# Kernel tuning notes

Measured on AMD Instinct MI355X. Metric: run time of the kernel, lower is better.

The kernel has to match this reference:

```python
import jax, jax.numpy as jnp
import numpy as np

N_NODES = 100000
N_ANGLES = 1000000
SCALAR_DIM = 128
ANGLE_ATTR_DIM = 2
HIDDEN = 64


def setup_inputs() -> dict:
    key = jax.random.key(0)
    ks = jax.random.split(key, 10)
    x = jax.random.normal(ks[0], (N_NODES, SCALAR_DIM), dtype=jnp.float32)
    triple_index = jax.random.randint(ks[1], (3, N_ANGLES), 0, N_NODES, dtype=jnp.int64)
    triple_attr = jax.random.normal(ks[2], (N_ANGLES, ANGLE_ATTR_DIM), dtype=jnp.float32)
    d_in = SCALAR_DIM * 2 + ANGLE_ATTR_DIM  # 258
    W1 = jax.random.normal(ks[3], (d_in, HIDDEN), dtype=jnp.float32) / np.sqrt(d_in)
    b1 = jnp.zeros((HIDDEN,), dtype=jnp.float32)
    W2 = jax.random.normal(ks[4], (HIDDEN, HIDDEN), dtype=jnp.float32) / np.sqrt(HIDDEN)
    b2 = jnp.zeros((HIDDEN,), dtype=jnp.float32)
    W3 = jax.random.normal(ks[5], (HIDDEN, SCALAR_DIM), dtype=jnp.float32) / np.sqrt(HIDDEN)
    b3 = jnp.zeros((SCALAR_DIM,), dtype=jnp.float32)
    # o3.Linear 128x0e -> 128x0e: bias-free dense linear with 1/sqrt(fan_in) norm
    Wout = jax.random.normal(ks[6], (SCALAR_DIM, SCALAR_DIM), dtype=jnp.float32) / np.sqrt(SCALAR_DIM)
    return {"x": x, "triple_index": triple_index, "triple_attr": triple_attr,
            "W1": W1, "b1": b1, "W2": W2, "b2": b2, "W3": W3, "b3": b3, "Wout": Wout}


def reference(x, triple_index, triple_attr, W1, b1, W2, b2, W3, b3, Wout):
    num_nodes = x.shape[0]
    x_scalar = x[:, :SCALAR_DIM]
    i, j, k = triple_index[0], triple_index[1], triple_index[2]
    # gather endpoints, concat with angle attrs: [E, 2*scalar_dim + 2]
    angle_input = jnp.concatenate([x_scalar[i], x_scalar[k], triple_attr], axis=-1)
    h = jax.nn.silu(angle_input @ W1 + b1)
    h = jax.nn.silu(h @ W2 + b2)
    msgs = h @ W3 + b3  # [E, scalar_dim]
    # scatter-mean by j
    sums = jax.ops.segment_sum(msgs, j, num_segments=num_nodes)
    cnts = jax.ops.segment_sum(jnp.ones((msgs.shape[0],), msgs.dtype), j, num_segments=num_nodes)
    aggr = sums / jnp.maximum(cnts, 1.0)[:, None]
    return aggr @ Wout
```

## Files before the change

kernel.cpp:

```cpp
#include <hip/hip_runtime.h>

#define NN 100000
#define NE 1000000
#define NBLK_SCAN 391

typedef float f4 __attribute__((ext_vector_type(4)));
typedef float f2 __attribute__((ext_vector_type(2)));
typedef _Float16 h8 __attribute__((ext_vector_type(8)));

__device__ __forceinline__ float silu(float v) {
    return v / (1.0f + __expf(-v));
}

#define O_SUMS   0
#define O_CNT    6400000
#define O_OFF    6500000
#define O_BSUM   6600000
#define O_PERM   6600512
#define O_XA     7600512
#define O_XB     10800512
#define O_W3W    14000512
#define O_W2T    14008832
#define O_W1TH   14010880
#define O_W1TR   14019072

#define HIST_B  3907
#define W3W_B   33
#define PREP0_B (HIST_B + W3W_B + 1 + 8)
#define NPRE_B  1563
#define MID_B   (NPRE_B + NBLK_SCAN)

__global__ __launch_bounds__(256) void k_prep0(
    const int* __restrict__ tj,
    const float* __restrict__ W1, const float* __restrict__ W2,
    const float* __restrict__ W3, const float* __restrict__ b3,
    const float* __restrict__ Wout,
    int* __restrict__ C, float* __restrict__ W3W, _Float16* __restrict__ W2t,
    _Float16* __restrict__ W1th, _Float16* __restrict__ W1tr) {
    const int b = blockIdx.x;
    const int t = threadIdx.x;
    if (b < HIST_B) {
        int e = b * 256 + t;
        if (e < NE) atomicAdd(&C[__builtin_nontemporal_load(tj + e)], 1);
    } else if (b < HIST_B + W3W_B) {
        const int row = (b - HIST_B) * 2 + (t >> 7);
        const int c = t & 127;
        if (row < 65) {
            const float* arow = (row < 64) ? (W3 + row * 128) : b3;
            float acc = 0.f;
            for (int d = 0; d < 128; ++d) acc += arow[d] * Wout[d * 128 + c];
            W3W[row * 128 + c] = acc;
        }
    } else if (b < HIST_B + W3W_B + 1) {
#pragma unroll
        for (int u = 0; u < 16; ++u) {
            const int idx = t * 16 + u;
            const int n = idx >> 6, k = idx & 63;
            W2t[idx] = (_Float16)W2[k * 64 + n];
        }
    } else {
        const int b0 = b - (HIST_B + W3W_B + 1);
#pragma unroll
        for (int u = 0; u < 8; ++u) {
            const int idx = b0 * 2048 + t * 8 + u;
            const int np = idx >> 7, k = idx & 127;
            const float wfull = W1[(k + ((np >= 64) ? 128 : 0)) * 64 + (np & 63)];
            const _Float16 wh = (_Float16)wfull;
            W1th[idx] = wh;
            W1tr[idx] = (_Float16)(wfull - (float)wh);
        }
    }
}

__global__ __launch_bounds__(256) void k_mid(
    const float* __restrict__ x,
    const _Float16* __restrict__ W1th, const _Float16* __restrict__ W1tr,
    _Float16* __restrict__ XA, _Float16* __restrict__ XB,
    const int* __restrict__ C, float* __restrict__ sums,
    int* __restrict__ offv, int* __restrict__ Bsum) {
    __shared__ _Float16 XOUT[2][64][72];
    __shared__ int s[256];
    const int b = blockIdx.x;
    const int t = threadIdx.x;
    if (b < NPRE_B) {
        const int n0 = b * 64;
        const int w = t >> 6;
        const int lane = t & 63;
        const int r15 = lane & 15, blk = lane >> 4;
        const int nodeRow = n0 + w * 16 + r15;
        const bool rowOK = nodeRow < NN;
        f4 accA[4], accB[4];
#pragma unroll
        for (int n = 0; n < 4; ++n) {
            accA[n] = (f4){0.f, 0.f, 0.f, 0.f};
            accB[n] = (f4){0.f, 0.f, 0.f, 0.f};
        }
#pragma unroll
        for (int kk = 0; kk < 4; ++kk) {
            f4 x0 = (f4){0.f, 0.f, 0.f, 0.f}, x1 = x0;
            if (rowOK) {
                const f4* xp = (const f4*)(x + (size_t)nodeRow * 128 + kk * 32 + blk * 8);
                x0 = xp[0];
                x1 = xp[1];
            }
            h8 xh, xr;
#pragma unroll
            for (int n = 0; n < 4; ++n) {
                xh[n] = (_Float16)x0[n];
                xr[n] = (_Float16)(x0[n] - (float)xh[n]);
                xh[4 + n] = (_Float16)x1[n];
                xr[4 + n] = (_Float16)(x1[n] - (float)xh[4 + n]);
            }
#pragma unroll
            for (int ncol = 0; ncol < 4; ++ncol) {
                const int nA = ncol * 16 + r15;
                const int koff = kk * 32 + blk * 8;
                h8 whA = *(const h8*)(W1th + nA * 128 + koff);
                h8 wrA = *(const h8*)(W1tr + nA * 128 + koff);
                accA[ncol] = __builtin_amdgcn_mfma_f32_16x16x32_f16(xh, whA, accA[ncol], 0, 0, 0);
                accA[ncol] = __builtin_amdgcn_mfma_f32_16x16x32_f16(xr, whA, accA[ncol], 0, 0, 0);
                accA[ncol] = __builtin_amdgcn_mfma_f32_16x16x32_f16(xh, wrA, accA[ncol], 0, 0, 0);
                h8 whB = *(const h8*)(W1th + (64 + nA) * 128 + koff);
                h8 wrB = *(const h8*)(W1tr + (64 + nA) * 128 + koff);
                accB[ncol] = __builtin_amdgcn_mfma_f32_16x16x32_f16(xh, whB, accB[ncol], 0, 0, 0);
                accB[ncol] = __builtin_amdgcn_mfma_f32_16x16x32_f16(xr, whB, accB[ncol], 0, 0, 0);
                accB[ncol] = __builtin_amdgcn_mfma_f32_16x16x32_f16(xh, wrB, accB[ncol], 0, 0, 0);
            }
        }
#pragma unroll
        for (int ncol = 0; ncol < 4; ++ncol)
#pragma unroll
            for (int reg = 0; reg < 4; ++reg) {
                const int row = w * 16 + blk * 4 + reg;
                XOUT[0][row][ncol * 16 + r15] = (_Float16)accA[ncol][reg];
                XOUT[1][row][ncol * 16 + r15] = (_Float16)accB[ncol][reg];
            }
        __syncthreads();
#pragma unroll
        for (int u = 0; u < 4; ++u) {
            const int idx = t + 256 * u;
            const int mat = idx >> 9;
            const int row = (idx >> 3) & 63;
            const int c8 = idx & 7;
            const int grow = n0 + row;
            if (grow < NN) {
                _Float16* dst = (mat ? XB : XA) + (size_t)grow * 64 + c8 * 8;
                *(h8*)dst = *(const h8*)&XOUT[mat][row][c8 * 8];
            }
        }
    } else {
        const int sb = b - NPRE_B;
        {
            f4* sz = (f4*)sums + (size_t)sb * 4096;
            const int cnt4 = min(4096, 1600000 - sb * 4096);
            for (int u = t; u < cnt4; u += 256) sz[u] = (f4){0.f, 0.f, 0.f, 0.f};
        }
        const int gid = sb * 256 + t;
        const int v = (gid < NN) ? C[gid] : 0;
        s[t] = v;
        __syncthreads();
        for (int off = 1; off < 256; off <<= 1) {
            int add = (t >= off) ? s[t - off] : 0;
            __syncthreads();
            s[t] += add;
            __syncthreads();
        }
        if (gid < NN) offv[gid] = s[t] - v;
        if (t == 255) Bsum[sb] = s[255];
    }
}

__global__ __launch_bounds__(256) void k_scatter(const int* __restrict__ tj,
                                                 const int* __restrict__ Bsum,
                                                 int* __restrict__ offv,
                                                 int* __restrict__ perm) {
    __shared__ int BpreS[NBLK_SCAN];
    const int t = threadIdx.x;
    const int w = t >> 6, lane = t & 63;
    if (w == 0) {
        int carry = 0;
        for (int base = 0; base < NBLK_SCAN; base += 64) {
            const int idx = base + lane;
            const int orig = (idx < NBLK_SCAN) ? Bsum[idx] : 0;
            int v = orig;
#pragma unroll
            for (int off = 1; off < 64; off <<= 1) {
                int u = __shfl_up(v, off, 64);
                if (lane >= off) v += u;
            }
            if (idx < NBLK_SCAN) BpreS[idx] = carry + v - orig;
            carry += __shfl(v, 63, 64);
        }
    }
    __syncthreads();
    const int e = blockIdx.x * 256 + t;
    if (e < NE) {
        const int j = __builtin_nontemporal_load(tj + e);
        const int p = BpreS[j >> 8] + atomicAdd(&offv[j], 1);
        perm[p] = e;
    }
}

__global__ __launch_bounds__(256, 8) void k_edge(
    const int* __restrict__ ti, const int* __restrict__ tj, const int* __restrict__ tk,
    const int* __restrict__ perm, const float* __restrict__ attr,
    const _Float16* __restrict__ XA, const _Float16* __restrict__ XB,
    const float* __restrict__ W1, const float* __restrict__ b1,
    const _Float16* __restrict__ W2t, const float* __restrict__ b2,
    float* __restrict__ sums) {
    __shared__ __align__(16) char SBraw[64 * 68 * 4];
    __shared__ int JL[64];
    __shared__ int RS[66];
    __shared__ int nruns_s;

    _Float16* H1h = (_Float16*)SBraw;
    float* M = (float*)SBraw;

    const int t = threadIdx.x;
    const int w = t >> 6;
    const int lane = t & 63;
    const int EB = blockIdx.x * 64;

    {
        const int el = t >> 2;
        const int q = t & 3;
        const int e = __builtin_nontemporal_load(perm + EB + el);
        const int i = __builtin_nontemporal_load(ti + e);
        const int k = __builtin_nontemporal_load(tk + e);
        if (q == 0) JL[el] = __builtin_nontemporal_load(tj + e);
        f2 at = __builtin_nontemporal_load((const f2*)attr + e);
        const _Float16* xa = XA + (size_t)i * 64 + q * 16;
        const _Float16* xb = XB + (size_t)k * 64 + q * 16;
        h8 va0 = ((const h8*)xa)[0], va1 = ((const h8*)xa)[1];
        h8 vb0 = ((const h8*)xb)[0], vb1 = ((const h8*)xb)[1];
        float fa[16], fb[16];
#pragma unroll
        for (int n = 0; n < 8; ++n) {
            fa[n] = (float)va0[n]; fa[8 + n] = (float)va1[n];
            fb[n] = (float)vb0[n]; fb[8 + n] = (float)vb1[n];
        }
        const float* c0 = W1 + 256 * 64 + q * 16;
        const float* c1 = W1 + 257 * 64 + q * 16;
        const float* bq = b1 + q * 16;
        _Float16 hrow[16];
#pragma unroll
        for (int m4 = 0; m4 < 4; ++m4) {
            f4 vc0 = ((const f4*)c0)[m4];
            f4 vc1 = ((const f4*)c1)[m4];
            f4 vbq = ((const f4*)bq)[m4];
#pragma unroll
            for (int n = 0; n < 4; ++n) {
                const int idx = m4 * 4 + n;
                float pre = fa[idx] + fb[idx] + at[0] * vc0[n] + at[1] * vc1[n] + vbq[n];
                hrow[idx] = (_Float16)silu(pre);
            }
        }
        h8 s0, s1;
#pragma unroll
        for (int n = 0; n < 8; ++n) { s0[n] = hrow[n]; s1[n] = hrow[8 + n]; }
        _Float16* row = H1h + el * 72 + q * 16;
        ((h8*)row)[0] = s0;
        ((h8*)row)[1] = s1;
    }
    __syncthreads();

    const int r15 = lane & 15;
    const int blk = lane >> 4;
    float h2v[16];
    {
        const _Float16* H1w = H1h + (w * 16) * 72;
        h8 a0 = *(const h8*)(H1w + r15 * 72 + blk * 8);
        h8 a1 = *(const h8*)(H1w + r15 * 72 + 32 + blk * 8);
#pragma unroll
        for (int ncol = 0; ncol < 4; ++ncol) {
            const _Float16* Wn = W2t + (ncol * 16 + r15) * 64 + blk * 8;
            h8 b0 = *(const h8*)(Wn);
            h8 b1v = *(const h8*)(Wn + 32);
            const float bc = b2[ncol * 16 + r15];
            f4 acc = {bc, bc, bc, bc};
            acc = __builtin_amdgcn_mfma_f32_16x16x32_f16(a0, b0, acc, 0, 0, 0);
            acc = __builtin_amdgcn_mfma_f32_16x16x32_f16(a1, b1v, acc, 0, 0, 0);
#pragma unroll
            for (int reg = 0; reg < 4; ++reg) h2v[ncol * 4 + reg] = silu(acc[reg]);
        }
    }
    __syncthreads();

#pragma unroll
    for (int ncol = 0; ncol < 4; ++ncol)
#pragma unroll
        for (int reg = 0; reg < 4; ++reg)
            M[(w * 16 + blk * 4 + reg) * 68 + ncol * 16 + r15] = h2v[ncol * 4 + reg];
    if (t < 64) {
        bool head = (t == 0) || (JL[t] != JL[t - 1]);
        unsigned long long mask = __ballot(head);
        if (head) {
            int rank = __popcll(mask & ((1ull << t) - 1ull));
            RS[rank] = t;
        }
        if (t == 0) {
            int nr = __popcll(mask);
            nruns_s = nr;
            RS[nr] = 64;
        }
    }
    __syncthreads();

    {
        const int col = t & 63;
        const int q4 = t >> 6;
        const int nr = nruns_s;
        for (int rid = q4; rid < nr; rid += 4) {
            const int s0 = RS[rid];
            const int s1 = RS[rid + 1];
            float a = 0.f;
            for (int rr = s0; rr < s1; ++rr) a += M[rr * 68 + col];
            atomicAdd(&sums[(size_t)JL[s0] * 64 + col], a);
        }
    }
}

__global__ __launch_bounds__(256) void k_out(const float* __restrict__ sums,
                                             const int* __restrict__ C,
                                             const float* __restrict__ W3W,
                                             float* __restrict__ out) {
    __shared__ float S[32][64];
    __shared__ float bs[32];
    const int t = threadIdx.x;
    const int n0 = blockIdx.x * 32;
    const f4* ss = (const f4*)(sums + (size_t)n0 * 64);
    f4* Ss = (f4*)&S[0][0];
#pragma unroll
    for (int q = 0; q < 2; ++q) {
        const int fidx = t + 256 * q;
        const int row = fidx >> 4;
        const int cn = C[n0 + row];
        const float sc = (cn > 0) ? 1.0f / (float)cn : 0.0f;
        f4 v = ss[fidx];
#pragma unroll
        for (int n = 0; n < 4; ++n) v[n] *= sc;
        Ss[fidx] = v;
    }
    if (t < 32) bs[t] = (C[n0 + t] > 0) ? 1.0f : 0.0f;
    __syncthreads();
    const int w = t >> 6, lane = t & 63;
    const float* bout = W3W + 64 * 128;
    float a0[8], a1[8];
#pragma unroll
    for (int m = 0; m < 8; ++m) { a0[m] = 0.f; a1[m] = 0.f; }
    for (int d = 0; d < 64; ++d) {
        float w0 = W3W[d * 128 + lane];
        float w1 = W3W[d * 128 + 64 + lane];
#pragma unroll
        for (int m = 0; m < 8; ++m) {
            float sv = S[w * 8 + m][d];
            a0[m] += sv * w0;
            a1[m] += sv * w1;
        }
    }
    const float bo0 = bout[lane], bo1 = bout[64 + lane];
#pragma unroll
    for (int m = 0; m < 8; ++m) {
        const int node = n0 + w * 8 + m;
        const float b = bs[w * 8 + m];
        out[(size_t)node * 128 + lane] = a0[m] + b * bo0;
        out[(size_t)node * 128 + 64 + lane] = a1[m] + b * bo1;
    }
}

extern "C" void kernel_launch(void* const* d_in, const int* in_sizes, int n_in,
                              void* d_out, int out_size, void* d_ws, size_t ws_size,
                              hipStream_t stream) {
    const float* x    = (const float*)d_in[0];
    const int*   idx  = (const int*)d_in[1];
    const float* attr = (const float*)d_in[2];
    const float* W1   = (const float*)d_in[3];
    const float* b1   = (const float*)d_in[4];
    const float* W2   = (const float*)d_in[5];
    const float* b2   = (const float*)d_in[6];
    const float* W3   = (const float*)d_in[7];
    const float* b3   = (const float*)d_in[8];
    const float* Wout = (const float*)d_in[9];
    float* out = (float*)d_out;

    const int* ti = idx;
    const int* tj = idx + NE;
    const int* tk = idx + 2 * NE;

    float* ws   = (float*)d_ws;
    float* sums = ws + O_SUMS;
    int*   C    = (int*)(ws + O_CNT);
    int*   offv = (int*)(ws + O_OFF);
    int*   Bsum = (int*)(ws + O_BSUM);
    int*   perm = (int*)(ws + O_PERM);
    _Float16* XA  = (_Float16*)(ws + O_XA);
    _Float16* XB  = (_Float16*)(ws + O_XB);
    float* W3W  = ws + O_W3W;
    _Float16* W2t  = (_Float16*)(ws + O_W2T);
    _Float16* W1th = (_Float16*)(ws + O_W1TH);
    _Float16* W1tr = (_Float16*)(ws + O_W1TR);

    hipMemsetAsync(C, 0, (size_t)NN * sizeof(int), stream);

    hipLaunchKernelGGL(k_prep0,   dim3(PREP0_B), dim3(256), 0, stream,
                       tj, W1, W2, W3, b3, Wout, C, W3W, W2t, W1th, W1tr);
    hipLaunchKernelGGL(k_mid,     dim3(MID_B), dim3(256), 0, stream,
                       x, W1th, W1tr, XA, XB, C, sums, offv, Bsum);
    hipLaunchKernelGGL(k_scatter, dim3(3907), dim3(256), 0, stream, tj, Bsum, offv, perm);
    hipLaunchKernelGGL(k_edge,    dim3(15625), dim3(256), 0, stream,
                       ti, tj, tk, perm, attr, XA, XB, W1, b1, W2t, b2, sums);
    hipLaunchKernelGGL(k_out,     dim3(3125), dim3(256), 0, stream, sums, C, W3W, out);
}
```

Baseline: 475.0 us.

## Scatter sorted edge payloads instead of permutation, split edge kernel launch

The scatter kernel now writes each edge's i, k and attribute pair as a packed int4 plus its j value into sorted order. The edge kernel therefore reads contiguous records instead of chasing a permutation into four separate arrays. The attribute and bias weights for the first layer are precomputed as fp16 and the edge kernel is launched as two halves. This removes the dependent random reads in the edge kernel, at the cost of extra scattered writes in k_scatter, an extra launch, and reduced precision on the attribute and bias weights.

```diff
diff --git a/kernel.cpp b/kernel.cpp
--- a/kernel.cpp
+++ b/kernel.cpp
@@ -16,32 +16,38 @@
 #define O_CNT    6400000
 #define O_OFF    6500000
 #define O_BSUM   6600000
-#define O_PERM   6600512
-#define O_XA     7600512
-#define O_XB     10800512
-#define O_W3W    14000512
-#define O_W2T    14008832
-#define O_W1TH   14010880
-#define O_W1TR   14019072
+#define O_TJS    6600512
+#define O_PL     7600512
+#define O_XA     11600512
+#define O_XB     14800512
+#define O_W3W    18000512
+#define O_W2T    18008832
+#define O_W1TH   18010880
+#define O_W1TR   18019072
+#define O_W1C16  18027264
 
 #define HIST_B  3907
 #define W3W_B   33
 #define PREP0_B (HIST_B + W3W_B + 1 + 8)
 #define NPRE_B  1563
 #define MID_B   (NPRE_B + NBLK_SCAN)
+#define EDGE_B1 7813
+#define EDGE_B2 7812
 
 __global__ __launch_bounds__(256) void k_prep0(
     const int* __restrict__ tj,
-    const float* __restrict__ W1, const float* __restrict__ W2,
+    const float* __restrict__ W1, const float* __restrict__ b1,
+    const float* __restrict__ W2,
     const float* __restrict__ W3, const float* __restrict__ b3,
     const float* __restrict__ Wout,
     int* __restrict__ C, float* __restrict__ W3W, _Float16* __restrict__ W2t,
-    _Float16* __restrict__ W1th, _Float16* __restrict__ W1tr) {
+    _Float16* __restrict__ W1th, _Float16* __restrict__ W1tr,
+    _Float16* __restrict__ W1C16) {
     const int b = blockIdx.x;
     const int t = threadIdx.x;
     if (b < HIST_B) {
         int e = b * 256 + t;
-        if (e < NE) atomicAdd(&C[__builtin_nontemporal_load(tj + e)], 1);
+        if (e < NE) atomicAdd(&C[tj[e]], 1);
     } else if (b < HIST_B + W3W_B) {
         const int row = (b - HIST_B) * 2 + (t >> 7);
         const int c = t & 127;
@@ -57,6 +63,11 @@
             const int idx = t * 16 + u;
             const int n = idx >> 6, k = idx & 63;
             W2t[idx] = (_Float16)W2[k * 64 + n];
+        }
+        if (t < 64) {
+            W1C16[t]        = (_Float16)W1[256 * 64 + t];
+            W1C16[64 + t]   = (_Float16)W1[257 * 64 + t];
+            W1C16[128 + t]  = (_Float16)b1[t];
         }
     } else {
         const int b0 = b - (HIST_B + W3W_B + 1);
@@ -170,10 +181,11 @@
     }
 }
 
-__global__ __launch_bounds__(256) void k_scatter(const int* __restrict__ tj,
-                                                 const int* __restrict__ Bsum,
-                                                 int* __restrict__ offv,
-                                                 int* __restrict__ perm) {
+__global__ __launch_bounds__(256) void k_scatter(
+    const int* __restrict__ ti, const int* __restrict__ tj, const int* __restrict__ tk,
+    const float* __restrict__ attr,
+    const int* __restrict__ Bsum, int* __restrict__ offv,
+    int* __restrict__ tjs, int4* __restrict__ PL4) {
     __shared__ int BpreS[NBLK_SCAN];
     const int t = threadIdx.x;
     const int w = t >> 6, lane = t & 63;
@@ -195,19 +207,20 @@
     __syncthreads();
     const int e = blockIdx.x * 256 + t;
     if (e < NE) {
-        const int j = __builtin_nontemporal_load(tj + e);
+        const int j = tj[e];
+        const f2 at = ((const f2*)attr)[e];
         const int p = BpreS[j >> 8] + atomicAdd(&offv[j], 1);
-        perm[p] = e;
+        tjs[p] = j;
+        PL4[p] = (int4){ti[e], tk[e], __float_as_int(at[0]), __float_as_int(at[1])};
     }
 }
 
 __global__ __launch_bounds__(256, 8) void k_edge(
-    const int* __restrict__ ti, const int* __restrict__ tj, const int* __restrict__ tk,
-    const int* __restrict__ perm, const float* __restrict__ attr,
+    const int* __restrict__ tjs, const int4* __restrict__ PL4,
     const _Float16* __restrict__ XA, const _Float16* __restrict__ XB,
-    const float* __restrict__ W1, const float* __restrict__ b1,
+    const _Float16* __restrict__ W1C16,
     const _Float16* __restrict__ W2t, const float* __restrict__ b2,
-    float* __restrict__ sums) {
+    float* __restrict__ sums, int blk0) {
     __shared__ __align__(16) char SBraw[64 * 68 * 4];
     __shared__ int JL[64];
     __shared__ int RS[66];
@@ -219,41 +232,36 @@
     const int t = threadIdx.x;
     const int w = t >> 6;
     const int lane = t & 63;
-    const int EB = blockIdx.x * 64;
+    const int EB = (blk0 + blockIdx.x) * 64;
 
     {
         const int el = t >> 2;
         const int q = t & 3;
-        const int e = __builtin_nontemporal_load(perm + EB + el);
-        const int i = __builtin_nontemporal_load(ti + e);
-        const int k = __builtin_nontemporal_load(tk + e);
-        if (q == 0) JL[el] = __builtin_nontemporal_load(tj + e);
-        f2 at = __builtin_nontemporal_load((const f2*)attr + e);
+        const int4 pl = PL4[EB + el];
+        const int i = pl.x;
+        const int k = pl.y;
+        if (q == 0) JL[el] = tjs[EB + el];
+        const float at0 = __int_as_float(pl.z);
+        const float at1 = __int_as_float(pl.w);
         const _Float16* xa = XA + (size_t)i * 64 + q * 16;
         const _Float16* xb = XB + (size_t)k * 64 + q * 16;
         h8 va0 = ((const h8*)xa)[0], va1 = ((const h8*)xa)[1];
         h8 vb0 = ((const h8*)xb)[0], vb1 = ((const h8*)xb)[1];
-        float fa[16], fb[16];
+        const _Float16* c0p = W1C16 + q * 16;
+        const _Float16* c1p = W1C16 + 64 + q * 16;
+        const _Float16* bqp = W1C16 + 128 + q * 16;
+        h8 c00 = ((const h8*)c0p)[0], c01 = ((const h8*)c0p)[1];
+        h8 c10 = ((const h8*)c1p)[0], c11 = ((const h8*)c1p)[1];
+        h8 bq0 = ((const h8*)bqp)[0], bq1 = ((const h8*)bqp)[1];
+        _Float16 hrow[16];
 #pragma unroll
         for (int n = 0; n < 8; ++n) {
-            fa[n] = (float)va0[n]; fa[8 + n] = (float)va1[n];
-            fb[n] = (float)vb0[n]; fb[8 + n] = (float)vb1[n];
-        }
-        const float* c0 = W1 + 256 * 64 + q * 16;
-        const float* c1 = W1 + 257 * 64 + q * 16;
-        const float* bq = b1 + q * 16;
-        _Float16 hrow[16];
-#pragma unroll
-        for (int m4 = 0; m4 < 4; ++m4) {
-            f4 vc0 = ((const f4*)c0)[m4];
-            f4 vc1 = ((const f4*)c1)[m4];
-            f4 vbq = ((const f4*)bq)[m4];
-#pragma unroll
-            for (int n = 0; n < 4; ++n) {
-                const int idx = m4 * 4 + n;
-                float pre = fa[idx] + fb[idx] + at[0] * vc0[n] + at[1] * vc1[n] + vbq[n];
-                hrow[idx] = (_Float16)silu(pre);
-            }
+            float pre0 = (float)va0[n] + (float)vb0[n]
+                       + at0 * (float)c00[n] + at1 * (float)c10[n] + (float)bq0[n];
+            float pre1 = (float)va1[n] + (float)vb1[n]
+                       + at0 * (float)c01[n] + at1 * (float)c11[n] + (float)bq1[n];
+            hrow[n] = (_Float16)silu(pre0);
+            hrow[8 + n] = (_Float16)silu(pre1);
         }
         h8 s0, s1;
 #pragma unroll
@@ -392,22 +400,27 @@
     int*   C    = (int*)(ws + O_CNT);
     int*   offv = (int*)(ws + O_OFF);
     int*   Bsum = (int*)(ws + O_BSUM);
-    int*   perm = (int*)(ws + O_PERM);
+    int*   tjs  = (int*)(ws + O_TJS);
+    int4*  PL4  = (int4*)(ws + O_PL);
     _Float16* XA  = (_Float16*)(ws + O_XA);
     _Float16* XB  = (_Float16*)(ws + O_XB);
     float* W3W  = ws + O_W3W;
-    _Float16* W2t  = (_Float16*)(ws + O_W2T);
-    _Float16* W1th = (_Float16*)(ws + O_W1TH);
-    _Float16* W1tr = (_Float16*)(ws + O_W1TR);
+    _Float16* W2t   = (_Float16*)(ws + O_W2T);
+    _Float16* W1th  = (_Float16*)(ws + O_W1TH);
+    _Float16* W1tr  = (_Float16*)(ws + O_W1TR);
+    _Float16* W1C16 = (_Float16*)(ws + O_W1C16);
 
     hipMemsetAsync(C, 0, (size_t)NN * sizeof(int), stream);
 
     hipLaunchKernelGGL(k_prep0,   dim3(PREP0_B), dim3(256), 0, stream,
-                       tj, W1, W2, W3, b3, Wout, C, W3W, W2t, W1th, W1tr);
+                       tj, W1, b1, W2, W3, b3, Wout, C, W3W, W2t, W1th, W1tr, W1C16);
     hipLaunchKernelGGL(k_mid,     dim3(MID_B), dim3(256), 0, stream,
                        x, W1th, W1tr, XA, XB, C, sums, offv, Bsum);
-    hipLaunchKernelGGL(k_scatter, dim3(3907), dim3(256), 0, stream, tj, Bsum, offv, perm);
-    hipLaunchKernelGGL(k_edge,    dim3(15625), dim3(256), 0, stream,
-                       ti, tj, tk, perm, attr, XA, XB, W1, b1, W2t, b2, sums);
+    hipLaunchKernelGGL(k_scatter, dim3(3907), dim3(256), 0, stream,
+                       ti, tj, tk, attr, Bsum, offv, tjs, PL4);
+    hipLaunchKernelGGL(k_edge,    dim3(EDGE_B1), dim3(256), 0, stream,
+                       tjs, PL4, XA, XB, W1C16, W2t, b2, sums, 0);
+    hipLaunchKernelGGL(k_edge,    dim3(EDGE_B2), dim3(256), 0, stream,
+                       tjs, PL4, XA, XB, W1C16, W2t, b2, sums, EDGE_B1);
     hipLaunchKernelGGL(k_out,     dim3(3125), dim3(256), 0, stream, sums, C, W3W, out);
 }
```

After: 401.1 us. 1.18x faster.
